# Performance work log

Measured on AMD Instinct MI355X. Metric: run time of the kernel, lower is better.

The kernel has to match this reference:

```python
import jax, jax.numpy as jnp
import numpy as np

B, S, D, H = 2, 2048, 1024, 16
DH = D // H  # dim_per_head = 64


def setup_inputs() -> dict:
    key = jax.random.key(0)
    ks = jax.random.split(key, 12)
    scale = 1.0 / np.sqrt(D)
    inp = {
        "key": jax.random.normal(ks[0], (B, S, D), jnp.float32),
        "value": jax.random.normal(ks[1], (B, S, D), jnp.float32),
        "query": jax.random.normal(ks[2], (B, S, D), jnp.float32),
        "mask": jax.random.randint(ks[3], (B, S, S), 0, 2) == 1,
        "Wq": jax.random.normal(ks[4], (D, D), jnp.float32) * scale,
        "bq": jnp.zeros((D,), jnp.float32),
        "Wk": jax.random.normal(ks[5], (D, D), jnp.float32) * scale,
        "bk": jnp.zeros((D,), jnp.float32),
        "Wv": jax.random.normal(ks[6], (D, D), jnp.float32) * scale,
        "bv": jnp.zeros((D,), jnp.float32),
        "Wo": jax.random.normal(ks[7], (D, D), jnp.float32) * scale,
        "bo": jnp.zeros((D,), jnp.float32),
    }
    return inp


def reference(key, value, query, mask, Wq, bq, Wk, bk, Wv, bv, Wo, bo):
    b, s, d = query.shape
    dh = d // H

    def split_heads(x):  # [b, s, d] -> [b, H, s, dh]
        return x.reshape(b, -1, H, dh).transpose(0, 2, 1, 3)

    q = split_heads(query @ Wq + bq) / jnp.sqrt(jnp.float32(dh))
    k = split_heads(key @ Wk + bk)
    v = split_heads(value @ Wv + bv)

    scores = jnp.einsum("bhqd,bhkd->bhqk", q, k)  # [b, H, s, s]
    scores = jnp.where(mask[:, None, :, :], jnp.float32(-1e18), scores)
    attn = jax.nn.softmax(scores, axis=-1)  # dropout is identity in eval
    ctx = jnp.einsum("bhqk,bhkd->bhqd", attn, v)
    ctx = ctx.transpose(0, 2, 1, 3).reshape(b, s, d)
    return ctx @ Wo + bo
```

## Files before the change

### kernel.cpp

```cpp
#include <hip/hip_runtime.h>
#include <hip/hip_bf16.h>

#define BATCH  2
#define SEQ    2048
#define DMODEL 1024
#define NHEAD  16
#define DHEAD  64
#define NTOK   (BATCH * SEQ)

using f32x4  = __attribute__((ext_vector_type(4))) float;
using f32x16 = __attribute__((ext_vector_type(16))) float;
using s16x4  = __attribute__((ext_vector_type(4))) short;
using s16x8  = __attribute__((ext_vector_type(8))) short;

__device__ __forceinline__ short f2bf(float f) {
  __hip_bfloat16 h = __float2bfloat16(f);
  return *(short*)&h;
}

__device__ __forceinline__ void gload_lds16(const short* g, short* l) {
  __builtin_amdgcn_global_load_lds(
      (const __attribute__((address_space(1))) void*)g,
      (__attribute__((address_space(3))) void*)l, 16, 0, 0);
}

__global__ __launch_bounds__(256) void prep_kernel(
    const float* __restrict__ Wq, const float* __restrict__ Wk,
    const float* __restrict__ Wv, const float* __restrict__ Wo,
    short* __restrict__ Wt,
    const float* __restrict__ Xq, const float* __restrict__ Xk,
    const float* __restrict__ Xv, short* __restrict__ Xb,
    const int* __restrict__ mask, unsigned long long* __restrict__ Mp) {
  __shared__ short tile[64][72];
  int bid = blockIdx.x, t = threadIdx.x;
  if (bid < 1024) {
    int z = bid >> 8, rem = bid & 255, x = rem & 15, y = rem >> 4;
    const float* W = z == 0 ? Wq : z == 1 ? Wk : z == 2 ? Wv : Wo;
    short* out = Wt + (size_t)z * DMODEL * DMODEL;
    int k0 = x * 64, n0 = y * 64;
#pragma unroll
    for (int i = 0; i < 4; ++i) {
      int idx = t + i * 256, row = idx >> 4, c4 = idx & 15;
      f32x4 v = *(const f32x4*)(W + (size_t)(k0 + row) * DMODEL + n0 + c4 * 4);
      s16x4 p;
      p[0] = f2bf(v[0]); p[1] = f2bf(v[1]); p[2] = f2bf(v[2]); p[3] = f2bf(v[3]);
      *(s16x4*)&tile[row][c4 * 4] = p;
    }
    __syncthreads();
#pragma unroll
    for (int i = 0; i < 2; ++i) {
      int idx = t + i * 256, nrow = idx >> 3, c8 = idx & 7;
      s16x8 p;
#pragma unroll
      for (int j = 0; j < 8; ++j) p[j] = tile[c8 * 8 + j][nrow];
      *(s16x8*)(out + (size_t)(n0 + nrow) * DMODEL + k0 + c8 * 8) = p;
    }
  } else if (bid < 7168) {
    int r = bid - 1024;
    int sel = r >> 11, bx = r & 2047;
    const float* src = sel == 0 ? Xq : sel == 1 ? Xk : Xv;
    size_t off = ((size_t)bx * 256 + t) * 8;
    f32x4 v0 = *(const f32x4*)(src + off);
    f32x4 v1 = *(const f32x4*)(src + off + 4);
    s16x8 p;
    p[0] = f2bf(v0[0]); p[1] = f2bf(v0[1]); p[2] = f2bf(v0[2]); p[3] = f2bf(v0[3]);
    p[4] = f2bf(v1[0]); p[5] = f2bf(v1[1]); p[6] = f2bf(v1[2]); p[7] = f2bf(v1[3]);
    *(s16x8*)(Xb + (size_t)sel * NTOK * DMODEL + off) = p;
  } else {
    int bx = bid - 7168;
    const int total_words = BATCH * SEQ * (SEQ / 64);
    int lane = t & 63;
    int wv = bx * 4 + (t >> 6);
    for (int w = wv; w < total_words; w += 4096) {
      int mv = mask[(size_t)w * 64 + lane];
      unsigned long long bits = __ballot(mv != 0);
      if (lane == 0) Mp[w] = bits;
    }
  }
}

__global__ __launch_bounds__(256) void proj_qkv_kernel(
    const short* __restrict__ Xb, const short* __restrict__ Wt,
    const float* __restrict__ bq, const float* __restrict__ bk,
    const float* __restrict__ bv, short* __restrict__ QKV) {
  __shared__ short As[3][128 * 32];
  __shared__ short Bs[3][128 * 32];
  int wg = blockIdx.x;
  int orig = (wg & 7) * 96 + (wg >> 3);
  int sel = orig >> 8;
  int rem = orig & 255;
  int mx = rem >> 3, ny = rem & 7;

  const short* X    = Xb + (size_t)sel * NTOK * DMODEL;
  const float* bias = sel == 0 ? bq : sel == 1 ? bk : bv;
  const short* Wsel = Wt + (size_t)sel * DMODEL * DMODEL;
  short* Obuf = QKV + (size_t)sel * ((size_t)BATCH * NHEAD * SEQ * DHEAD);
  const float scale = sel == 0 ? 0.18033688011111793f : 1.0f;

  int m0 = mx * 128, n0 = ny * 128;
  int t = threadIdx.x, wid = t >> 6, lane = t & 63;
  int lr = lane & 15, lg = lane >> 4;
  int wr = wid >> 1, wc = wid & 1;
  f32x4 acc[4][4] = {};

  const int gr0 = t >> 2, gc0 = (t & 3) << 3;
  const short* Ax0 = X + (size_t)(m0 + gr0) * DMODEL + gc0;
  const short* Ax1 = Ax0 + (size_t)64 * DMODEL;
  const short* Bw0 = Wsel + (size_t)(n0 + gr0) * DMODEL + gc0;
  const short* Bw1 = Bw0 + (size_t)64 * DMODEL;
  const int lofs0 = (t & ~63) << 3, lofs1 = lofs0 + 256 * 8;

#define STAGEQ(bufi, k0s) {                                                   \
    gload_lds16(Ax0 + (k0s), &As[bufi][0] + lofs0);                           \
    gload_lds16(Ax1 + (k0s), &As[bufi][0] + lofs1);                           \
    gload_lds16(Bw0 + (k0s), &Bs[bufi][0] + lofs0);                           \
    gload_lds16(Bw1 + (k0s), &Bs[bufi][0] + lofs1); }

  STAGEQ(0, 0);
  STAGEQ(1, 32);

  int cb = 0;
  for (int kt = 0; kt < 32; ++kt) {
    if (kt + 1 < 32) { asm volatile("s_waitcnt vmcnt(4)" ::: "memory"); }
    else             { asm volatile("s_waitcnt vmcnt(0)" ::: "memory"); }
    __builtin_amdgcn_sched_barrier(0);
    __builtin_amdgcn_s_barrier();
    __builtin_amdgcn_sched_barrier(0);
    int st = cb + 2; if (st > 2) st -= 3;
    if (kt + 2 < 32) STAGEQ(st, (kt + 2) * 32);

    s16x8 afr[4], bfr[4];
#pragma unroll
    for (int mi = 0; mi < 4; ++mi)
      afr[mi] = *(const s16x8*)(&As[cb][0] + (wr * 64 + mi * 16 + lr) * 32 + lg * 8);
#pragma unroll
    for (int ni = 0; ni < 4; ++ni)
      bfr[ni] = *(const s16x8*)(&Bs[cb][0] + (wc * 64 + ni * 16 + lr) * 32 + lg * 8);
    __builtin_amdgcn_s_setprio(1);
#pragma unroll
    for (int mi = 0; mi < 4; ++mi)
#pragma unroll
      for (int ni = 0; ni < 4; ++ni)
        acc[mi][ni] = __builtin_amdgcn_mfma_f32_16x16x32_bf16(
            afr[mi], bfr[ni], acc[mi][ni], 0, 0, 0);
    __builtin_amdgcn_s_setprio(0);
    cb = (cb == 2) ? 0 : cb + 1;
  }
#undef STAGEQ

  if (sel == 2) {
    int bq_ = m0 >> 11;
    int s0 = (m0 & (SEQ - 1)) + wr * 64 + lg * 4;
#pragma unroll
    for (int mi = 0; mi < 4; ++mi)
#pragma unroll
      for (int ni = 0; ni < 4; ++ni) {
        int n = n0 + wc * 64 + ni * 16 + lr;
        float bv_ = bias[n];
        int h = n >> 6, d = n & 63;
        s16x4 pk;
#pragma unroll
        for (int r = 0; r < 4; ++r) pk[r] = f2bf(acc[mi][ni][r] + bv_);
        *(s16x4*)&Obuf[((size_t)(bq_ * NHEAD + h) * DHEAD + d) * SEQ
                       + s0 + mi * 16] = pk;
      }
  } else {
#pragma unroll
    for (int mi = 0; mi < 4; ++mi)
#pragma unroll
      for (int ni = 0; ni < 4; ++ni) {
        int n = n0 + wc * 64 + ni * 16 + lr;
        float bv_ = bias[n];
        int h = n >> 6, d = n & 63;
#pragma unroll
        for (int r = 0; r < 4; ++r) {
          int m = m0 + wr * 64 + mi * 16 + lg * 4 + r;
          int b = m >> 11, s = m & (SEQ - 1);
          float val = (acc[mi][ni][r] + bv_) * scale;
          Obuf[((size_t)(b * NHEAD + h) * SEQ + s) * DHEAD + d] = f2bf(val);
        }
      }
  }
}

__global__ __launch_bounds__(256) void attn_kernel(
    const short* __restrict__ Qb, const short* __restrict__ Kb,
    const short* __restrict__ VbT, const unsigned long long* __restrict__ Mp,
    short* __restrict__ Ctx) {
  __shared__ short Ks[3][64 * 64];
  __shared__ short Vt[3][64 * 64];
  int wg = blockIdx.x;
  int orig = (wg & 7) * 64 + (wg >> 3);
  int bh = orig >> 4, qt = orig & 15;
  int b = bh >> 4, h = bh & 15;
  int q0 = qt * 128;
  int t = threadIdx.x, wid = t >> 6, lane = t & 63;
  int ql = lane & 31, hi = lane >> 5;
  int qrow = q0 + wid * 32 + ql;

  const short* Qp = Qb + ((size_t)bh * SEQ + qrow) * DHEAD + hi * 8;
  s16x8 qf[4];
#pragma unroll
  for (int ds = 0; ds < 4; ++ds) qf[ds] = *(const s16x8*)(Qp + ds * 16);

  const short* KbB = Kb + (size_t)bh * SEQ * DHEAD;
  const short* VtB = VbT + (size_t)bh * DHEAD * SEQ;

  const int srow = lane >> 3;
  const int schunk = ((lane & 7) ^ srow) * 8;

  int offK[4];
#pragma unroll
  for (int j = 0; j < 4; ++j)
    offK[j] = ql * 64 + (((j * 2 + hi) ^ (ql & 7)) << 3);
  int offVa[4], offVb[4];
#pragma unroll
  for (int m = 0; m < 4; ++m) {
    offVa[m] = ql * 64 + (((m * 2)     ^ (ql & 7)) << 3) + 4 * hi;
    offVb[m] = ql * 64 + (((m * 2 + 1) ^ (ql & 7)) << 3) + 4 * hi;
  }

  float m_run = -1e30f, l_run = 0.f;
  f32x16 oacc0 = {}, oacc1 = {};
  s16x8 pPack[4];
  s16x8 vA[4], vB[4];

  const unsigned long long* mrow = Mp + ((size_t)b * SEQ + qrow) * (SEQ / 64);

#define STAGE(bufi, k0s)                                                      \
  {                                                                           \
    _Pragma("unroll")                                                         \
    for (int i = 0; i < 2; ++i) {                                             \
      int rbase = wid * 16 + i * 8;                                           \
      gload_lds16(KbB + (size_t)((k0s) + rbase + srow) * DHEAD + schunk,      \
                  &Ks[bufi][rbase * 64]);                                     \
      gload_lds16(VtB + (size_t)(rbase + srow) * SEQ + (k0s) + schunk,        \
                  &Vt[bufi][rbase * 64]);                                     \
    }                                                                         \
  }

  unsigned long long mwq0 = mrow[0], mwq1 = mrow[1];
  STAGE(0, 0);
  STAGE(1, 64);

  int cb = 0;
  for (int kt = 0; kt < 32; ++kt) {
    if (kt + 1 < 32) { asm volatile("s_waitcnt vmcnt(4)" ::: "memory"); }
    else             { asm volatile("s_waitcnt vmcnt(0)" ::: "memory"); }
    __builtin_amdgcn_sched_barrier(0);
    __builtin_amdgcn_s_barrier();
    __builtin_amdgcn_sched_barrier(0);
    int st = cb + 2; if (st > 2) st -= 3;
    if (kt + 2 < 32) STAGE(st, (kt + 2) * 64);
    unsigned long long mw_cur = mwq0;
    mwq0 = mwq1;
    if (kt + 2 < 32) mwq1 = mrow[kt + 2];

    const short* KsC = Ks[cb];
    const short* VtC = Vt[cb];

    f32x16 sf0 = {}, sf1 = {};
    __builtin_amdgcn_s_setprio(1);
#pragma unroll
    for (int ds = 0; ds < 4; ++ds) {
      s16x8 k0 = *(const s16x8*)&KsC[offK[ds]];
      s16x8 k1 = *(const s16x8*)&KsC[offK[ds] + 2048];
      sf0 = __builtin_amdgcn_mfma_f32_32x32x16_bf16(k0, qf[ds], sf0, 0, 0, 0);
      sf1 = __builtin_amdgcn_mfma_f32_32x32x16_bf16(k1, qf[ds], sf1, 0, 0, 0);
    }
    if (kt > 0) {
#pragma unroll
      for (int m = 0; m < 4; ++m) {
        oacc0 = __builtin_amdgcn_mfma_f32_32x32x16_bf16(pPack[m], vA[m], oacc0, 0, 0, 0);
        oacc1 = __builtin_amdgcn_mfma_f32_32x32x16_bf16(pPack[m], vB[m], oacc1, 0, 0, 0);
      }
    }
    __builtin_amdgcn_s_setprio(0);

#pragma unroll
    for (int m = 0; m < 4; ++m) {
      union { s16x4 q[2]; s16x8 v; } v0, v1;
      v0.q[0] = *(const s16x4*)&VtC[offVa[m]];
      v0.q[1] = *(const s16x4*)&VtC[offVb[m]];
      v1.q[0] = *(const s16x4*)&VtC[offVa[m] + 2048];
      v1.q[1] = *(const s16x4*)&VtC[offVb[m] + 2048];
      vA[m] = v0.v;
      vB[m] = v1.v;
    }

    unsigned h0 = ((unsigned)mw_cur) >> (hi << 2);
    unsigned h1 = ((unsigned)(mw_cur >> 32)) >> (hi << 2);
#pragma unroll
    for (int r = 0; r < 16; ++r) {
      const int c = (r & 3) + 8 * (r >> 2);
      if ((h0 >> c) & 1u) sf0[r] = -1e30f;
      if ((h1 >> c) & 1u) sf1[r] = -1e30f;
    }
    float tm = sf0[0];
#pragma unroll
    for (int r = 1; r < 16; ++r) tm = fmaxf(tm, sf0[r]);
#pragma unroll
    for (int r = 0; r < 16; ++r) tm = fmaxf(tm, sf1[r]);

    bool small = __all(tm <= m_run + 8.0f);
    if (!small) {
      float tmx = fmaxf(tm, __shfl_xor(tm, 32, 64));
      float mnew = fmaxf(m_run, tmx);
      float scl = __builtin_amdgcn_exp2f(m_run - mnew);
      m_run = mnew;
      l_run *= scl;
#pragma unroll
      for (int r = 0; r < 16; ++r) {
        float s_ = __shfl(scl, (r & 3) + 8 * (r >> 2) + 4 * hi, 64);
        oacc0[r] *= s_;
        oacc1[r] *= s_;
      }
    }

    float ss = 0.f;
#pragma unroll
    for (int r = 0; r < 16; ++r) {
      sf0[r] = __builtin_amdgcn_exp2f(sf0[r] - m_run);
      sf1[r] = __builtin_amdgcn_exp2f(sf1[r] - m_run);
      ss += sf0[r] + sf1[r];
    }
    l_run += ss;

#pragma unroll
    for (int m = 0; m < 4; ++m) {
      const int base = (m & 1) * 8;
      s16x8 pa;
#pragma unroll
      for (int e = 0; e < 8; ++e)
        pa[e] = f2bf(m < 2 ? sf0[base + e] : sf1[base + e]);
      pPack[m] = pa;
    }

    asm volatile("s_waitcnt lgkmcnt(0)" ::: "memory");
    __builtin_amdgcn_sched_barrier(0);
    cb = (cb == 2) ? 0 : cb + 1;
  }
#undef STAGE

  __builtin_amdgcn_s_setprio(1);
#pragma unroll
  for (int m = 0; m < 4; ++m) {
    oacc0 = __builtin_amdgcn_mfma_f32_32x32x16_bf16(pPack[m], vA[m], oacc0, 0, 0, 0);
    oacc1 = __builtin_amdgcn_mfma_f32_32x32x16_bf16(pPack[m], vB[m], oacc1, 0, 0, 0);
  }
  __builtin_amdgcn_s_setprio(0);

  float l_tot = l_run + __shfl_xor(l_run, 32, 64);
#pragma unroll
  for (int r = 0; r < 16; ++r) {
    int c = (r & 3) + 8 * (r >> 2) + 4 * hi;
    float linv = 1.0f / __shfl(l_tot, c, 64);
    int q_ = q0 + wid * 32 + c;
    size_t base = ((size_t)b * SEQ + q_) * DMODEL + h * DHEAD + ql;
    Ctx[base] = f2bf(oacc0[r] * linv);
    Ctx[base + 32] = f2bf(oacc1[r] * linv);
  }
}

__global__ __launch_bounds__(256) void proj_out_kernel(
    const short* __restrict__ Ctx, const short* __restrict__ Wot,
    const float* __restrict__ bo, float* __restrict__ Out) {
  __shared__ short As[3][128 * 32];
  __shared__ short Bs[3][128 * 32];
  int wg = blockIdx.x;
  int orig = (wg & 7) * 32 + (wg >> 3);
  int mx = orig >> 3, ny = orig & 7;
  int m0 = mx * 128, n0 = ny * 128;
  int t = threadIdx.x, wid = t >> 6, lane = t & 63;
  int lr = lane & 15, lg = lane >> 4;
  int wr = wid >> 1, wc = wid & 1;
  f32x4 acc[4][4] = {};

  const int gr0 = t >> 2, gc0 = (t & 3) << 3;
  const short* Actx0 = Ctx + (size_t)(m0 + gr0) * DMODEL + gc0;
  const short* Actx1 = Actx0 + (size_t)64 * DMODEL;
  const short* Bwo0 = Wot + (size_t)(n0 + gr0) * DMODEL + gc0;
  const short* Bwo1 = Bwo0 + (size_t)64 * DMODEL;
  const int lofs0 = (t & ~63) << 3, lofs1 = lofs0 + 256 * 8;

#define STAGE_PO(bufi, k0s) {                                                 \
    gload_lds16(Actx0 + (k0s), &As[bufi][0] + lofs0);                         \
    gload_lds16(Actx1 + (k0s), &As[bufi][0] + lofs1);                         \
    gload_lds16(Bwo0 + (k0s), &Bs[bufi][0] + lofs0);                          \
    gload_lds16(Bwo1 + (k0s), &Bs[bufi][0] + lofs1); }

  STAGE_PO(0, 0);
  STAGE_PO(1, 32);

  int cb = 0;
  for (int kt = 0; kt < 32; ++kt) {
    if (kt + 1 < 32) { asm volatile("s_waitcnt vmcnt(4)" ::: "memory"); }
    else             { asm volatile("s_waitcnt vmcnt(0)" ::: "memory"); }
    __builtin_amdgcn_sched_barrier(0);
    __builtin_amdgcn_s_barrier();
    __builtin_amdgcn_sched_barrier(0);
    int st = cb + 2; if (st > 2) st -= 3;
    if (kt + 2 < 32) STAGE_PO(st, (kt + 2) * 32);

    s16x8 afr[4], bfr[4];
#pragma unroll
    for (int mi = 0; mi < 4; ++mi)
      afr[mi] = *(const s16x8*)(&As[cb][0] + (wr * 64 + mi * 16 + lr) * 32 + lg * 8);
#pragma unroll
    for (int ni = 0; ni < 4; ++ni)
      bfr[ni] = *(const s16x8*)(&Bs[cb][0] + (wc * 64 + ni * 16 + lr) * 32 + lg * 8);
    __builtin_amdgcn_s_setprio(1);
#pragma unroll
    for (int mi = 0; mi < 4; ++mi)
#pragma unroll
      for (int ni = 0; ni < 4; ++ni)
        acc[mi][ni] = __builtin_amdgcn_mfma_f32_16x16x32_bf16(
            afr[mi], bfr[ni], acc[mi][ni], 0, 0, 0);
    __builtin_amdgcn_s_setprio(0);
    cb = (cb == 2) ? 0 : cb + 1;
  }
#undef STAGE_PO

#pragma unroll
  for (int mi = 0; mi < 4; ++mi)
#pragma unroll
    for (int ni = 0; ni < 4; ++ni) {
      int n = n0 + wc * 64 + ni * 16 + lr;
      float bv_ = bo[n];
#pragma unroll
      for (int r = 0; r < 4; ++r) {
        int m = m0 + wr * 64 + mi * 16 + lg * 4 + r;
        Out[(size_t)m * DMODEL + n] = acc[mi][ni][r] + bv_;
      }
    }
}

extern "C" void kernel_launch(void* const* d_in, const int* in_sizes, int n_in,
                              void* d_out, int out_size, void* d_ws, size_t ws_size,
                              hipStream_t stream) {
  const float* key_in   = (const float*)d_in[0];
  const float* value_in = (const float*)d_in[1];
  const float* query_in = (const float*)d_in[2];
  const int*   mask     = (const int*)d_in[3];
  const float* Wq = (const float*)d_in[4];
  const float* bq = (const float*)d_in[5];
  const float* Wk = (const float*)d_in[6];
  const float* bk = (const float*)d_in[7];
  const float* Wv = (const float*)d_in[8];
  const float* bv = (const float*)d_in[9];
  const float* Wo = (const float*)d_in[10];
  const float* bo = (const float*)d_in[11];
  float* out = (float*)d_out;

  short* ws = (short*)d_ws;
  const size_t WSZ   = (size_t)DMODEL * DMODEL;
  const size_t QKVSZ = (size_t)BATCH * NHEAD * SEQ * DHEAD;
  short* Wt  = ws;
  short* QKV = ws + 4 * WSZ;
  short* Qb  = QKV;
  short* Kb  = QKV + QKVSZ;
  short* VbT = QKV + 2 * QKVSZ;
  short* Xb  = ws + 4 * WSZ + 3 * QKVSZ;
  short* Ctx = Xb;
  unsigned long long* Mp = (unsigned long long*)d_out;

  prep_kernel<<<dim3(8192), 256, 0, stream>>>(
      Wq, Wk, Wv, Wo, Wt, query_in, key_in, value_in, Xb, mask, Mp);
  proj_qkv_kernel<<<dim3(768), 256, 0, stream>>>(Xb, Wt, bq, bk, bv, QKV);
  attn_kernel<<<dim3(512), 256, 0, stream>>>(Qb, Kb, VbT, Mp, Ctx);
  proj_out_kernel<<<dim3(256), 256, 0, stream>>>(Ctx, Wt + 3 * WSZ, bo, out);
}
```

Measured before the change: 162.9 us.

## Split attention key range in two halves and merge partial softmax results

The attention kernel now splits each query tile's 32 key tiles into two halves processed by separate workgroups, doubling the grid to 1024 blocks. Each half writes a normalized partial output plus its running max and sum, and a new merge kernel combines them into the context buffer. The K/V staging ring shrinks from triple to double buffering with a full vmcnt(0) wait, and launch bounds request 4 blocks per CU. This targets low occupancy on a 512-block grid, at the cost of an extra kernel launch, extra global traffic for the partials, and less load latency hiding.

Result: slower. 269.3 us (+65.3%).

```diff
diff --git a/kernel.cpp b/kernel.cpp
--- a/kernel.cpp
+++ b/kernel.cpp
@@ -7,6 +7,7 @@
 #define NHEAD  16
 #define DHEAD  64
 #define NTOK   (BATCH * SEQ)
+#define NROWS  (BATCH * NHEAD * SEQ)
 
 using f32x4  = __attribute__((ext_vector_type(4))) float;
 using f32x16 = __attribute__((ext_vector_type(16))) float;
@@ -16,6 +17,12 @@
 __device__ __forceinline__ short f2bf(float f) {
   __hip_bfloat16 h = __float2bfloat16(f);
   return *(short*)&h;
+}
+
+__device__ __forceinline__ float bf2f(short s) {
+  union { unsigned u; float f; } v;
+  v.u = ((unsigned)(unsigned short)s) << 16;
+  return v.f;
 }
 
 __device__ __forceinline__ void gload_lds16(const short* g, short* l) {
@@ -183,20 +190,21 @@
   }
 }
 
-__global__ __launch_bounds__(256) void attn_kernel(
+__global__ __launch_bounds__(256, 4) void attn_kernel(
     const short* __restrict__ Qb, const short* __restrict__ Kb,
     const short* __restrict__ VbT, const unsigned long long* __restrict__ Mp,
-    short* __restrict__ Ctx) {
-  __shared__ short Ks[3][64 * 64];
-  __shared__ short Vt[3][64 * 64];
+    short* __restrict__ Opart, float2* __restrict__ lmbuf) {
+  __shared__ short Ks[2][64 * 64];
+  __shared__ short Vt[2][64 * 64];
   int wg = blockIdx.x;
-  int orig = (wg & 7) * 64 + (wg >> 3);
-  int bh = orig >> 4, qt = orig & 15;
-  int b = bh >> 4, h = bh & 15;
+  int orig = (wg & 7) * 128 + (wg >> 3);
+  int bh = orig >> 5, qt = (orig >> 1) & 15, half = orig & 1;
+  int b = bh >> 4;
   int q0 = qt * 128;
   int t = threadIdx.x, wid = t >> 6, lane = t & 63;
   int ql = lane & 31, hi = lane >> 5;
   int qrow = q0 + wid * 32 + ql;
+  const int kbeg = half * 16, kend = kbeg + 16;
 
   const short* Qp = Qb + ((size_t)bh * SEQ + qrow) * DHEAD + hi * 8;
   s16x8 qf[4];
@@ -239,25 +247,21 @@
     }                                                                         \
   }
 
-  unsigned long long mwq0 = mrow[0], mwq1 = mrow[1];
-  STAGE(0, 0);
-  STAGE(1, 64);
-
-  int cb = 0;
-  for (int kt = 0; kt < 32; ++kt) {
-    if (kt + 1 < 32) { asm volatile("s_waitcnt vmcnt(4)" ::: "memory"); }
-    else             { asm volatile("s_waitcnt vmcnt(0)" ::: "memory"); }
+  unsigned long long mwq0 = mrow[kbeg];
+  STAGE(0, kbeg * 64);
+
+  int cur = 0;
+  for (int kt = kbeg; kt < kend; ++kt) {
+    asm volatile("s_waitcnt vmcnt(0)" ::: "memory");
     __builtin_amdgcn_sched_barrier(0);
     __builtin_amdgcn_s_barrier();
     __builtin_amdgcn_sched_barrier(0);
-    int st = cb + 2; if (st > 2) st -= 3;
-    if (kt + 2 < 32) STAGE(st, (kt + 2) * 64);
+    if (kt + 1 < kend) STAGE(cur ^ 1, (kt + 1) * 64);
     unsigned long long mw_cur = mwq0;
-    mwq0 = mwq1;
-    if (kt + 2 < 32) mwq1 = mrow[kt + 2];
-
-    const short* KsC = Ks[cb];
-    const short* VtC = Vt[cb];
+    if (kt + 1 < kend) mwq0 = mrow[kt + 1];
+
+    const short* KsC = Ks[cur];
+    const short* VtC = Vt[cur];
 
     f32x16 sf0 = {}, sf1 = {};
     __builtin_amdgcn_s_setprio(1);
@@ -268,7 +272,7 @@
       sf0 = __builtin_amdgcn_mfma_f32_32x32x16_bf16(k0, qf[ds], sf0, 0, 0, 0);
       sf1 = __builtin_amdgcn_mfma_f32_32x32x16_bf16(k1, qf[ds], sf1, 0, 0, 0);
     }
-    if (kt > 0) {
+    if (kt > kbeg) {
 #pragma unroll
       for (int m = 0; m < 4; ++m) {
         oacc0 = __builtin_amdgcn_mfma_f32_32x32x16_bf16(pPack[m], vA[m], oacc0, 0, 0, 0);
@@ -338,7 +342,7 @@
 
     asm volatile("s_waitcnt lgkmcnt(0)" ::: "memory");
     __builtin_amdgcn_sched_barrier(0);
-    cb = (cb == 2) ? 0 : cb + 1;
+    cur ^= 1;
   }
 #undef STAGE
 
@@ -351,15 +355,43 @@
   __builtin_amdgcn_s_setprio(0);
 
   float l_tot = l_run + __shfl_xor(l_run, 32, 64);
+  if (hi == 0) {
+    float2 v; v.x = m_run; v.y = l_tot;
+    lmbuf[(size_t)half * NROWS + (size_t)bh * SEQ + qrow] = v;
+  }
+  short* Op = Opart + (size_t)half * NROWS * DHEAD;
 #pragma unroll
   for (int r = 0; r < 16; ++r) {
     int c = (r & 3) + 8 * (r >> 2) + 4 * hi;
     float linv = 1.0f / __shfl(l_tot, c, 64);
     int q_ = q0 + wid * 32 + c;
-    size_t base = ((size_t)b * SEQ + q_) * DMODEL + h * DHEAD + ql;
-    Ctx[base] = f2bf(oacc0[r] * linv);
-    Ctx[base + 32] = f2bf(oacc1[r] * linv);
-  }
+    size_t base = ((size_t)bh * SEQ + q_) * DHEAD + ql;
+    Op[base] = f2bf(oacc0[r] * linv);
+    Op[base + 32] = f2bf(oacc1[r] * linv);
+  }
+}
+
+__global__ __launch_bounds__(256) void merge_kernel(
+    const short* __restrict__ Opart, const float2* __restrict__ lmbuf,
+    short* __restrict__ Ctx) {
+  int row = blockIdx.x * 32 + (threadIdx.x >> 3);
+  int dc = (threadIdx.x & 7) * 8;
+  float2 lm1 = lmbuf[row];
+  float2 lm2 = lmbuf[NROWS + row];
+  float m = fmaxf(lm1.x, lm2.x);
+  float w1 = lm1.y * __builtin_amdgcn_exp2f(lm1.x - m);
+  float w2 = lm2.y * __builtin_amdgcn_exp2f(lm2.x - m);
+  float inv = 1.0f / (w1 + w2);
+  float a1 = w1 * inv, a2 = w2 * inv;
+  s16x8 o1 = *(const s16x8*)(Opart + (size_t)row * DHEAD + dc);
+  s16x8 o2 = *(const s16x8*)(Opart + (size_t)NROWS * DHEAD + (size_t)row * DHEAD + dc);
+  int bh = row >> 11, q = row & (SEQ - 1);
+  int b = bh >> 4, h = bh & 15;
+  s16x8 o;
+#pragma unroll
+  for (int j = 0; j < 8; ++j)
+    o[j] = f2bf(a1 * bf2f(o1[j]) + a2 * bf2f(o2[j]));
+  *(s16x8*)(Ctx + ((size_t)(b * SEQ + q) * DMODEL) + h * DHEAD + dc) = o;
 }
 
 __global__ __launch_bounds__(256) void proj_out_kernel(
@@ -462,11 +494,14 @@
   short* VbT = QKV + 2 * QKVSZ;
   short* Xb  = ws + 4 * WSZ + 3 * QKVSZ;
   short* Ctx = Xb;
+  short* Opart = Xb + QKVSZ;
   unsigned long long* Mp = (unsigned long long*)d_out;
+  float2* lmbuf = (float2*)((char*)d_out + (1 << 20));
 
   prep_kernel<<<dim3(8192), 256, 0, stream>>>(
       Wq, Wk, Wv, Wo, Wt, query_in, key_in, value_in, Xb, mask, Mp);
   proj_qkv_kernel<<<dim3(768), 256, 0, stream>>>(Xb, Wt, bq, bk, bv, QKV);
-  attn_kernel<<<dim3(512), 256, 0, stream>>>(Qb, Kb, VbT, Mp, Ctx);
+  attn_kernel<<<dim3(1024), 256, 0, stream>>>(Qb, Kb, VbT, Mp, Opart, lmbuf);
+  merge_kernel<<<dim3(2048), 256, 0, stream>>>(Opart, lmbuf, Ctx);
   proj_out_kernel<<<dim3(256), 256, 0, stream>>>(Ctx, Wt + 3 * WSZ, bo, out);
 }
```

## Fuse fp32-to-bf16 activation conversion into the QKV projection GEMM

Applied to the files above, without the earlier changes.

The separate prep pass that converted query/key/value from fp32 to bf16 into a workspace buffer is removed. The QKV projection kernel now loads fp32 activation tiles into registers one k-step ahead, converts them to bf16 and writes them to LDS, while the weight tiles keep using async global-to-LDS loads. This is meant to drop a full read-write-reread round trip of the activations through memory and one large grid of prep blocks. In exchange, each GEMM block reads twice as many activation bytes (fp32), redundantly across column tiles. It also adds conversion ALU work and register pressure, and the pipeline now mixes register-staged and direct-to-LDS loads with hand-tuned vmcnt waits.

New measurement: 166.1 us. Within noise of the previous version (+2.0%).

```diff
diff --git a/kernel.cpp b/kernel.cpp
--- a/kernel.cpp
+++ b/kernel.cpp
@@ -28,8 +28,6 @@
     const float* __restrict__ Wq, const float* __restrict__ Wk,
     const float* __restrict__ Wv, const float* __restrict__ Wo,
     short* __restrict__ Wt,
-    const float* __restrict__ Xq, const float* __restrict__ Xk,
-    const float* __restrict__ Xv, short* __restrict__ Xb,
     const int* __restrict__ mask, unsigned long long* __restrict__ Mp) {
   __shared__ short tile[64][72];
   int bid = blockIdx.x, t = threadIdx.x;
@@ -55,19 +53,8 @@
       for (int j = 0; j < 8; ++j) p[j] = tile[c8 * 8 + j][nrow];
       *(s16x8*)(out + (size_t)(n0 + nrow) * DMODEL + k0 + c8 * 8) = p;
     }
-  } else if (bid < 7168) {
-    int r = bid - 1024;
-    int sel = r >> 11, bx = r & 2047;
-    const float* src = sel == 0 ? Xq : sel == 1 ? Xk : Xv;
-    size_t off = ((size_t)bx * 256 + t) * 8;
-    f32x4 v0 = *(const f32x4*)(src + off);
-    f32x4 v1 = *(const f32x4*)(src + off + 4);
-    s16x8 p;
-    p[0] = f2bf(v0[0]); p[1] = f2bf(v0[1]); p[2] = f2bf(v0[2]); p[3] = f2bf(v0[3]);
-    p[4] = f2bf(v1[0]); p[5] = f2bf(v1[1]); p[6] = f2bf(v1[2]); p[7] = f2bf(v1[3]);
-    *(s16x8*)(Xb + (size_t)sel * NTOK * DMODEL + off) = p;
   } else {
-    int bx = bid - 7168;
+    int bx = bid - 1024;
     const int total_words = BATCH * SEQ * (SEQ / 64);
     int lane = t & 63;
     int wv = bx * 4 + (t >> 6);
@@ -80,7 +67,8 @@
 }
 
 __global__ __launch_bounds__(256) void proj_qkv_kernel(
-    const short* __restrict__ Xb, const short* __restrict__ Wt,
+    const float* __restrict__ Xq, const float* __restrict__ Xk,
+    const float* __restrict__ Xv, const short* __restrict__ Wt,
     const float* __restrict__ bq, const float* __restrict__ bk,
     const float* __restrict__ bv, short* __restrict__ QKV) {
   __shared__ short As[3][128 * 32];
@@ -91,7 +79,7 @@
   int rem = orig & 255;
   int mx = rem >> 3, ny = rem & 7;
 
-  const short* X    = Xb + (size_t)sel * NTOK * DMODEL;
+  const float* X    = sel == 0 ? Xq : sel == 1 ? Xk : Xv;
   const float* bias = sel == 0 ? bq : sel == 1 ? bk : bv;
   const short* Wsel = Wt + (size_t)sel * DMODEL * DMODEL;
   short* Obuf = QKV + (size_t)sel * ((size_t)BATCH * NHEAD * SEQ * DHEAD);
@@ -104,30 +92,47 @@
   f32x4 acc[4][4] = {};
 
   const int gr0 = t >> 2, gc0 = (t & 3) << 3;
-  const short* Ax0 = X + (size_t)(m0 + gr0) * DMODEL + gc0;
-  const short* Ax1 = Ax0 + (size_t)64 * DMODEL;
+  const float* Arow0 = X + (size_t)(m0 + gr0) * DMODEL + gc0;
+  const float* Arow1 = Arow0 + (size_t)64 * DMODEL;
+  const int aofs0 = gr0 * 32 + gc0, aofs1 = aofs0 + 64 * 32;
   const short* Bw0 = Wsel + (size_t)(n0 + gr0) * DMODEL + gc0;
   const short* Bw1 = Bw0 + (size_t)64 * DMODEL;
-  const int lofs0 = (t & ~63) << 3, lofs1 = lofs0 + 256 * 8;
-
-#define STAGEQ(bufi, k0s) {                                                   \
-    gload_lds16(Ax0 + (k0s), &As[bufi][0] + lofs0);                           \
-    gload_lds16(Ax1 + (k0s), &As[bufi][0] + lofs1);                           \
-    gload_lds16(Bw0 + (k0s), &Bs[bufi][0] + lofs0);                           \
-    gload_lds16(Bw1 + (k0s), &Bs[bufi][0] + lofs1); }
-
-  STAGEQ(0, 0);
-  STAGEQ(1, 32);
+  const int bofs0 = (t & ~63) << 3, bofs1 = bofs0 + 256 * 8;
+
+  f32x4 a00, a01, a10, a11;
+#define LOADA(k0s) {                                                          \
+    a00 = *(const f32x4*)(Arow0 + (k0s));                                     \
+    a01 = *(const f32x4*)(Arow0 + (k0s) + 4);                                 \
+    a10 = *(const f32x4*)(Arow1 + (k0s));                                     \
+    a11 = *(const f32x4*)(Arow1 + (k0s) + 4); }
+#define STAGEB(bufi, k0s) {                                                   \
+    gload_lds16(Bw0 + (k0s), &Bs[bufi][0] + bofs0);                           \
+    gload_lds16(Bw1 + (k0s), &Bs[bufi][0] + bofs1); }
+#define WRITEA(bufi) {                                                        \
+    s16x8 p0, p1;                                                             \
+    p0[0]=f2bf(a00[0]); p0[1]=f2bf(a00[1]); p0[2]=f2bf(a00[2]); p0[3]=f2bf(a00[3]); \
+    p0[4]=f2bf(a01[0]); p0[5]=f2bf(a01[1]); p0[6]=f2bf(a01[2]); p0[7]=f2bf(a01[3]); \
+    p1[0]=f2bf(a10[0]); p1[1]=f2bf(a10[1]); p1[2]=f2bf(a10[2]); p1[3]=f2bf(a10[3]); \
+    p1[4]=f2bf(a11[0]); p1[5]=f2bf(a11[1]); p1[6]=f2bf(a11[2]); p1[7]=f2bf(a11[3]); \
+    *(s16x8*)(&As[bufi][0] + aofs0) = p0;                                     \
+    *(s16x8*)(&As[bufi][0] + aofs1) = p1; }
+
+  LOADA(0);
+  asm volatile("s_waitcnt vmcnt(0)" ::: "memory");
+  WRITEA(0);
+  STAGEB(0, 0);
+  STAGEB(1, 32);
+  asm volatile("s_waitcnt vmcnt(2)" ::: "memory");
 
   int cb = 0;
   for (int kt = 0; kt < 32; ++kt) {
-    if (kt + 1 < 32) { asm volatile("s_waitcnt vmcnt(4)" ::: "memory"); }
-    else             { asm volatile("s_waitcnt vmcnt(0)" ::: "memory"); }
+    asm volatile("s_waitcnt lgkmcnt(0)" ::: "memory");
     __builtin_amdgcn_sched_barrier(0);
     __builtin_amdgcn_s_barrier();
     __builtin_amdgcn_sched_barrier(0);
+    if (kt + 1 < 32) LOADA((kt + 1) * 32);
     int st = cb + 2; if (st > 2) st -= 3;
-    if (kt + 2 < 32) STAGEQ(st, (kt + 2) * 32);
+    if (kt + 2 < 32) STAGEB(st, (kt + 2) * 32);
 
     s16x8 afr[4], bfr[4];
 #pragma unroll
@@ -144,9 +149,18 @@
         acc[mi][ni] = __builtin_amdgcn_mfma_f32_16x16x32_bf16(
             afr[mi], bfr[ni], acc[mi][ni], 0, 0, 0);
     __builtin_amdgcn_s_setprio(0);
+
+    if (kt + 1 < 32) {
+      if (kt + 2 < 32) { asm volatile("s_waitcnt vmcnt(2)" ::: "memory"); }
+      else             { asm volatile("s_waitcnt vmcnt(0)" ::: "memory"); }
+      int wa = cb + 1; if (wa > 2) wa -= 3;
+      WRITEA(wa);
+    }
     cb = (cb == 2) ? 0 : cb + 1;
   }
-#undef STAGEQ
+#undef LOADA
+#undef STAGEB
+#undef WRITEA
 
   if (sel == 2) {
     int bq_ = m0 >> 11;
@@ -460,13 +474,12 @@
   short* Qb  = QKV;
   short* Kb  = QKV + QKVSZ;
   short* VbT = QKV + 2 * QKVSZ;
-  short* Xb  = ws + 4 * WSZ + 3 * QKVSZ;
-  short* Ctx = Xb;
+  short* Ctx = ws + 4 * WSZ + 3 * QKVSZ;
   unsigned long long* Mp = (unsigned long long*)d_out;
 
-  prep_kernel<<<dim3(8192), 256, 0, stream>>>(
-      Wq, Wk, Wv, Wo, Wt, query_in, key_in, value_in, Xb, mask, Mp);
-  proj_qkv_kernel<<<dim3(768), 256, 0, stream>>>(Xb, Wt, bq, bk, bv, QKV);
+  prep_kernel<<<dim3(2048), 256, 0, stream>>>(Wq, Wk, Wv, Wo, Wt, mask, Mp);
+  proj_qkv_kernel<<<dim3(768), 256, 0, stream>>>(
+      query_in, key_in, value_in, Wt, bq, bk, bv, QKV);
   attn_kernel<<<dim3(512), 256, 0, stream>>>(Qb, Kb, VbT, Mp, Ctx);
   proj_out_kernel<<<dim3(256), 256, 0, stream>>>(Ctx, Wt + 3 * WSZ, bo, out);
 }
```

## Stage 128-key tiles with double buffering in attention kernel

Applied to the files above, without the earlier changes.

Replaces the triple-buffered 64-key K/V staging with double-buffered 128-key tiles, halving the number of barriers and waits per head. Each staged tile is processed as two 64-key sub-steps, and the mask words are loaded directly per group instead of being prefetched. The V tile layout changes to 128-wide rows with a new swizzle. Prefetch depth drops from two tiles ahead to one, and vmcnt(0) now waits for all loads each iteration, so load latency may be exposed more than before.

Result: slower. 186.8 us (+14.6%).

```diff
diff --git a/kernel.cpp b/kernel.cpp
--- a/kernel.cpp
+++ b/kernel.cpp
@@ -187,8 +187,8 @@
     const short* __restrict__ Qb, const short* __restrict__ Kb,
     const short* __restrict__ VbT, const unsigned long long* __restrict__ Mp,
     short* __restrict__ Ctx) {
-  __shared__ short Ks[3][64 * 64];
-  __shared__ short Vt[3][64 * 64];
+  __shared__ short Ks[2][128 * 64];
+  __shared__ short Vt[2][64 * 128];
   int wg = blockIdx.x;
   int orig = (wg & 7) * 64 + (wg >> 3);
   int bh = orig >> 4, qt = orig & 15;
@@ -206,8 +206,9 @@
   const short* KbB = Kb + (size_t)bh * SEQ * DHEAD;
   const short* VtB = VbT + (size_t)bh * DHEAD * SEQ;
 
-  const int srow = lane >> 3;
-  const int schunk = ((lane & 7) ^ srow) * 8;
+  const int srowK = lane >> 3;
+  const int schunkK = ((lane & 7) ^ srowK) * 8;
+  const int srow4 = lane >> 4;
 
   int offK[4];
 #pragma unroll
@@ -216,8 +217,8 @@
   int offVa[4], offVb[4];
 #pragma unroll
   for (int m = 0; m < 4; ++m) {
-    offVa[m] = ql * 64 + (((m * 2)     ^ (ql & 7)) << 3) + 4 * hi;
-    offVb[m] = ql * 64 + (((m * 2 + 1) ^ (ql & 7)) << 3) + 4 * hi;
+    offVa[m] = ql * 128 + (((m * 2)     ^ (ql & 7)) << 3) + 4 * hi;
+    offVb[m] = ql * 128 + (((m * 2 + 1) ^ (ql & 7)) << 3) + 4 * hi;
   }
 
   float m_run = -1e30f, l_run = 0.f;
@@ -227,120 +228,125 @@
 
   const unsigned long long* mrow = Mp + ((size_t)b * SEQ + qrow) * (SEQ / 64);
 
-#define STAGE(bufi, k0s)                                                      \
+#define STAGE128(bufi, grp)                                                   \
   {                                                                           \
     _Pragma("unroll")                                                         \
-    for (int i = 0; i < 2; ++i) {                                             \
-      int rbase = wid * 16 + i * 8;                                           \
-      gload_lds16(KbB + (size_t)((k0s) + rbase + srow) * DHEAD + schunk,      \
-                  &Ks[bufi][rbase * 64]);                                     \
-      gload_lds16(VtB + (size_t)(rbase + srow) * SEQ + (k0s) + schunk,        \
-                  &Vt[bufi][rbase * 64]);                                     \
+    for (int i = 0; i < 4; ++i) {                                             \
+      int krb = wid * 32 + i * 8;                                             \
+      gload_lds16(KbB + (size_t)((grp) * 128 + krb + srowK) * DHEAD + schunkK,\
+                  &Ks[bufi][krb * 64]);                                       \
+      int vrb = wid * 16 + i * 4;                                             \
+      int vrow7 = ((i & 1) << 2) + srow4;                                     \
+      int vch = (lane & 8) | ((lane & 7) ^ vrow7);                            \
+      gload_lds16(VtB + (size_t)(vrb + srow4) * SEQ + (grp) * 128 + vch * 8,  \
+                  &Vt[bufi][vrb * 128]);                                      \
     }                                                                         \
   }
 
-  unsigned long long mwq0 = mrow[0], mwq1 = mrow[1];
-  STAGE(0, 0);
-  STAGE(1, 64);
+  STAGE128(0, 0);
 
   int cb = 0;
-  for (int kt = 0; kt < 32; ++kt) {
-    if (kt + 1 < 32) { asm volatile("s_waitcnt vmcnt(4)" ::: "memory"); }
-    else             { asm volatile("s_waitcnt vmcnt(0)" ::: "memory"); }
+  for (int g = 0; g < 16; ++g) {
+    asm volatile("s_waitcnt vmcnt(0)" ::: "memory");
     __builtin_amdgcn_sched_barrier(0);
     __builtin_amdgcn_s_barrier();
     __builtin_amdgcn_sched_barrier(0);
-    int st = cb + 2; if (st > 2) st -= 3;
-    if (kt + 2 < 32) STAGE(st, (kt + 2) * 64);
-    unsigned long long mw_cur = mwq0;
-    mwq0 = mwq1;
-    if (kt + 2 < 32) mwq1 = mrow[kt + 2];
+    if (g + 1 < 16) STAGE128(cb ^ 1, g + 1);
+    unsigned long long mwA = mrow[2 * g];
+    unsigned long long mwB = mrow[2 * g + 1];
 
     const short* KsC = Ks[cb];
     const short* VtC = Vt[cb];
 
-    f32x16 sf0 = {}, sf1 = {};
-    __builtin_amdgcn_s_setprio(1);
-#pragma unroll
-    for (int ds = 0; ds < 4; ++ds) {
-      s16x8 k0 = *(const s16x8*)&KsC[offK[ds]];
-      s16x8 k1 = *(const s16x8*)&KsC[offK[ds] + 2048];
-      sf0 = __builtin_amdgcn_mfma_f32_32x32x16_bf16(k0, qf[ds], sf0, 0, 0, 0);
-      sf1 = __builtin_amdgcn_mfma_f32_32x32x16_bf16(k1, qf[ds], sf1, 0, 0, 0);
+#pragma unroll
+    for (int su = 0; su < 2; ++su) {
+      const short* KsS = KsC + su * 4096;
+      const short* VtS = VtC + su * 64;
+      unsigned long long mw_cur = su ? mwB : mwA;
+
+      f32x16 sf0 = {}, sf1 = {};
+      __builtin_amdgcn_s_setprio(1);
+#pragma unroll
+      for (int ds = 0; ds < 4; ++ds) {
+        s16x8 k0 = *(const s16x8*)&KsS[offK[ds]];
+        s16x8 k1 = *(const s16x8*)&KsS[offK[ds] + 2048];
+        sf0 = __builtin_amdgcn_mfma_f32_32x32x16_bf16(k0, qf[ds], sf0, 0, 0, 0);
+        sf1 = __builtin_amdgcn_mfma_f32_32x32x16_bf16(k1, qf[ds], sf1, 0, 0, 0);
+      }
+      if (g > 0 || su == 1) {
+#pragma unroll
+        for (int m = 0; m < 4; ++m) {
+          oacc0 = __builtin_amdgcn_mfma_f32_32x32x16_bf16(pPack[m], vA[m], oacc0, 0, 0, 0);
+          oacc1 = __builtin_amdgcn_mfma_f32_32x32x16_bf16(pPack[m], vB[m], oacc1, 0, 0, 0);
+        }
+      }
+      __builtin_amdgcn_s_setprio(0);
+
+#pragma unroll
+      for (int m = 0; m < 4; ++m) {
+        union { s16x4 q[2]; s16x8 v; } v0, v1;
+        v0.q[0] = *(const s16x4*)&VtS[offVa[m]];
+        v0.q[1] = *(const s16x4*)&VtS[offVb[m]];
+        v1.q[0] = *(const s16x4*)&VtS[offVa[m] + 4096];
+        v1.q[1] = *(const s16x4*)&VtS[offVb[m] + 4096];
+        vA[m] = v0.v;
+        vB[m] = v1.v;
+      }
+
+      unsigned h0 = ((unsigned)mw_cur) >> (hi << 2);
+      unsigned h1 = ((unsigned)(mw_cur >> 32)) >> (hi << 2);
+#pragma unroll
+      for (int r = 0; r < 16; ++r) {
+        const int c = (r & 3) + 8 * (r >> 2);
+        if ((h0 >> c) & 1u) sf0[r] = -1e30f;
+        if ((h1 >> c) & 1u) sf1[r] = -1e30f;
+      }
+      float tm = sf0[0];
+#pragma unroll
+      for (int r = 1; r < 16; ++r) tm = fmaxf(tm, sf0[r]);
+#pragma unroll
+      for (int r = 0; r < 16; ++r) tm = fmaxf(tm, sf1[r]);
+
+      bool small = __all(tm <= m_run + 8.0f);
+      if (!small) {
+        float tmx = fmaxf(tm, __shfl_xor(tm, 32, 64));
+        float mnew = fmaxf(m_run, tmx);
+        float scl = __builtin_amdgcn_exp2f(m_run - mnew);
+        m_run = mnew;
+        l_run *= scl;
+#pragma unroll
+        for (int r = 0; r < 16; ++r) {
+          float s_ = __shfl(scl, (r & 3) + 8 * (r >> 2) + 4 * hi, 64);
+          oacc0[r] *= s_;
+          oacc1[r] *= s_;
+        }
+      }
+
+      float ss = 0.f;
+#pragma unroll
+      for (int r = 0; r < 16; ++r) {
+        sf0[r] = __builtin_amdgcn_exp2f(sf0[r] - m_run);
+        sf1[r] = __builtin_amdgcn_exp2f(sf1[r] - m_run);
+        ss += sf0[r] + sf1[r];
+      }
+      l_run += ss;
+
+#pragma unroll
+      for (int m = 0; m < 4; ++m) {
+        const int base = (m & 1) * 8;
+        s16x8 pa;
+#pragma unroll
+        for (int e = 0; e < 8; ++e)
+          pa[e] = f2bf(m < 2 ? sf0[base + e] : sf1[base + e]);
+        pPack[m] = pa;
+      }
     }
-    if (kt > 0) {
-#pragma unroll
-      for (int m = 0; m < 4; ++m) {
-        oacc0 = __builtin_amdgcn_mfma_f32_32x32x16_bf16(pPack[m], vA[m], oacc0, 0, 0, 0);
-        oacc1 = __builtin_amdgcn_mfma_f32_32x32x16_bf16(pPack[m], vB[m], oacc1, 0, 0, 0);
-      }
-    }
-    __builtin_amdgcn_s_setprio(0);
-
-#pragma unroll
-    for (int m = 0; m < 4; ++m) {
-      union { s16x4 q[2]; s16x8 v; } v0, v1;
-      v0.q[0] = *(const s16x4*)&VtC[offVa[m]];
-      v0.q[1] = *(const s16x4*)&VtC[offVb[m]];
-      v1.q[0] = *(const s16x4*)&VtC[offVa[m] + 2048];
-      v1.q[1] = *(const s16x4*)&VtC[offVb[m] + 2048];
-      vA[m] = v0.v;
-      vB[m] = v1.v;
-    }
-
-    unsigned h0 = ((unsigned)mw_cur) >> (hi << 2);
-    unsigned h1 = ((unsigned)(mw_cur >> 32)) >> (hi << 2);
-#pragma unroll
-    for (int r = 0; r < 16; ++r) {
-      const int c = (r & 3) + 8 * (r >> 2);
-      if ((h0 >> c) & 1u) sf0[r] = -1e30f;
-      if ((h1 >> c) & 1u) sf1[r] = -1e30f;
-    }
-    float tm = sf0[0];
-#pragma unroll
-    for (int r = 1; r < 16; ++r) tm = fmaxf(tm, sf0[r]);
-#pragma unroll
-    for (int r = 0; r < 16; ++r) tm = fmaxf(tm, sf1[r]);
-
-    bool small = __all(tm <= m_run + 8.0f);
-    if (!small) {
-      float tmx = fmaxf(tm, __shfl_xor(tm, 32, 64));
-      float mnew = fmaxf(m_run, tmx);
-      float scl = __builtin_amdgcn_exp2f(m_run - mnew);
-      m_run = mnew;
-      l_run *= scl;
-#pragma unroll
-      for (int r = 0; r < 16; ++r) {
-        float s_ = __shfl(scl, (r & 3) + 8 * (r >> 2) + 4 * hi, 64);
-        oacc0[r] *= s_;
-        oacc1[r] *= s_;
-      }
-    }
-
-    float ss = 0.f;
-#pragma unroll
-    for (int r = 0; r < 16; ++r) {
-      sf0[r] = __builtin_amdgcn_exp2f(sf0[r] - m_run);
-      sf1[r] = __builtin_amdgcn_exp2f(sf1[r] - m_run);
-      ss += sf0[r] + sf1[r];
-    }
-    l_run += ss;
-
-#pragma unroll
-    for (int m = 0; m < 4; ++m) {
-      const int base = (m & 1) * 8;
-      s16x8 pa;
-#pragma unroll
-      for (int e = 0; e < 8; ++e)
-        pa[e] = f2bf(m < 2 ? sf0[base + e] : sf1[base + e]);
-      pPack[m] = pa;
-    }
 
     asm volatile("s_waitcnt lgkmcnt(0)" ::: "memory");
     __builtin_amdgcn_sched_barrier(0);
-    cb = (cb == 2) ? 0 : cb + 1;
-  }
-#undef STAGE
+    cb ^= 1;
+  }
+#undef STAGE128
 
   __builtin_amdgcn_s_setprio(1);
 #pragma unroll
@@ -386,7 +392,7 @@
 #define STAGE_PO(bufi, k0s) {                                                 \
     gload_lds16(Actx0 + (k0s), &As[bufi][0] + lofs0);                         \
     gload_lds16(Actx1 + (k0s), &As[bufi][0] + lofs1);                         \
-    gload_lds16(Bwo0 + (k0s), &Bs[bufi][0] + lofs0);                          \
+    gload_lds16(Bwo0 + (k0s), &Bs[bufi][0] + lofs0);                         \
     gload_lds16(Bwo1 + (k0s), &Bs[bufi][0] + lofs1); }
 
   STAGE_PO(0, 0);
```
